# Kernel optimization log

Measured on AMD Instinct MI355X. Metric: run time of the kernel, lower is better.

Reference implementation:

```python
import jax, jax.numpy as jnp
import numpy as np

B, N, D = 2, 2048, 1024
H = 16
HD = D // H


def setup_inputs() -> dict:
    key = jax.random.key(0)
    ks = jax.random.split(key, 10)
    s = 1.0 / np.sqrt(D)
    return {
        "x": jax.random.normal(ks[0], (B, N, D), dtype=jnp.float32),
        "B_gaussian": jax.random.normal(ks[1], (B, N, N), dtype=jnp.float32),
        "Wq": jax.random.normal(ks[2], (D, D), dtype=jnp.float32) * s,
        "bq": jnp.zeros((D,), dtype=jnp.float32),
        "Wk": jax.random.normal(ks[3], (D, D), dtype=jnp.float32) * s,
        "bk": jnp.zeros((D,), dtype=jnp.float32),
        "Wv": jax.random.normal(ks[4], (D, D), dtype=jnp.float32) * s,
        "bv": jnp.zeros((D,), dtype=jnp.float32),
        "Wo": jax.random.normal(ks[5], (D, D), dtype=jnp.float32) * s,
        "bo": jnp.zeros((D,), dtype=jnp.float32),
        "lam": jnp.float32(0.5),
    }


def reference(x, B_gaussian, Wq, bq, Wk, bk, Wv, bv, Wo, bo, lam):
    b, n, d = x.shape
    # project and split heads: [b, h, n, hd]
    def heads(W, bias):
        return (x @ W + bias).reshape(b, n, H, HD).transpose(0, 2, 1, 3)
    q = heads(Wq, bq)
    k = heads(Wk, bk)
    v = heads(Wv, bv)
    scale = 1.0 / np.sqrt(HD)
    # scores [b, h, n, n] with Gaussian bias broadcast across heads
    scores = jnp.einsum("bhid,bhjd->bhij", q, k) * scale + lam * B_gaussian[:, None, :, :]
    w = jax.nn.softmax(scores, axis=-1)
    out = jnp.einsum("bhij,bhjd->bhid", w, v)
    out = out.transpose(0, 2, 1, 3).reshape(b, n, d)
    return out @ Wo + bo
```

## Files before the change

kernel.cpp:

```cpp
#include <hip/hip_runtime.h>
#include <math.h>
#include <stdint.h>

namespace {
constexpr int kB  = 2;
constexpr int kN  = 2048;
constexpr int kD  = 1024;
constexpr int kH  = 16;
constexpr int kM  = kB * kN;
}

typedef __attribute__((ext_vector_type(8))) _Float16 f16x8;
typedef __attribute__((ext_vector_type(2))) __fp16   fp16x2;
typedef __attribute__((ext_vector_type(4))) float    f32x4;

__device__ __forceinline__ void split16(float v, _Float16& h, _Float16& l) {
    h = (_Float16)v;
    l = (_Float16)(v - (float)h);
}

__device__ __forceinline__ void gl2lds16(const _Float16* g, _Float16* l) {
    __builtin_amdgcn_global_load_lds(
        (const __attribute__((address_space(1))) void*)g,
        (__attribute__((address_space(3))) void*)l, 16, 0, 0);
}

__global__ __launch_bounds__(256)
void cvt16(const float* __restrict__ x, _Float16* __restrict__ o)
{
    const size_t i = ((size_t)blockIdx.x * 256 + threadIdx.x) * 8;
    const float4 a = *(const float4*)(x + i);
    const float4 b = *(const float4*)(x + i + 4);
    _Float16 h[8] = {(_Float16)a.x, (_Float16)a.y, (_Float16)a.z, (_Float16)a.w,
                     (_Float16)b.x, (_Float16)b.y, (_Float16)b.z, (_Float16)b.w};
    *(uint4*)(o + i) = *(uint4*)h;
}

__global__ __launch_bounds__(256)
void bgprep(const float* __restrict__ Bg, const float* __restrict__ lam_p,
            _Float16* __restrict__ bgC)
{
    const int t    = blockIdx.x * 256 + threadIdx.x;
    const int lane = t & 63;
    const int i16  = (t >> 6) & 127;
    const int jt   = (t >> 13) & 31;
    const int b    = t >> 18;
    const int q    = lane >> 4;
    const int m    = lane & 15;
    const float c  = lam_p[0] * 8.0f;
    const float* src = Bg + ((size_t)b * kN + i16 * 16 + m) * kN + jt * 64 + q * 4;
    _Float16 h[16];
#pragma unroll
    for (int js = 0; js < 4; ++js) {
        const float4 v = *(const float4*)(src + js * 16);
        h[js * 4 + 0] = (_Float16)(c * v.x);
        h[js * 4 + 1] = (_Float16)(c * v.y);
        h[js * 4 + 2] = (_Float16)(c * v.z);
        h[js * 4 + 3] = (_Float16)(c * v.w);
    }
    _Float16* dst = bgC + (size_t)t * 16;
    *(uint4*)(dst)     = *(uint4*)(h);
    *(uint4*)(dst + 8) = *(uint4*)(h + 8);
}

__global__ __launch_bounds__(256)
void wcvt_t(const float* __restrict__ W, _Float16* __restrict__ Ot)
{
    __shared__ float sT[64][69];
    const int tid = threadIdx.x;
    const int k0 = blockIdx.x << 6;
    const int n0 = blockIdx.y << 6;
#pragma unroll
    for (int rep = 0; rep < 4; ++rep) {
        const int idx = tid + (rep << 8);
        const int kr  = idx >> 4;
        const int c4  = (idx & 15) << 2;
        const float4 v = *(const float4*)(W + (size_t)(k0 + kr) * kD + n0 + c4);
        sT[kr][c4 + 0] = v.x; sT[kr][c4 + 1] = v.y;
        sT[kr][c4 + 2] = v.z; sT[kr][c4 + 3] = v.w;
    }
    __syncthreads();
#pragma unroll
    for (int rep = 0; rep < 2; ++rep) {
        const int slot = tid + (rep << 8);
        const int n  = slot >> 3;
        const int k8 = (slot & 7) << 3;
        _Float16 h8[8];
#pragma unroll
        for (int j = 0; j < 8; ++j) h8[j] = (_Float16)sT[k8 + j][n];
        *(uint4*)(Ot + (size_t)(n0 + n) * kD + k0 + k8) = *(uint4*)h8;
    }
}

__global__ __launch_bounds__(256)
void wsplit_t(const float* __restrict__ W, _Float16* __restrict__ Oh,
              _Float16* __restrict__ Ol)
{
    __shared__ float sT[64][69];
    const int tid = threadIdx.x;
    const int k0 = blockIdx.x << 6;
    const int n0 = blockIdx.y << 6;
#pragma unroll
    for (int rep = 0; rep < 4; ++rep) {
        const int idx = tid + (rep << 8);
        const int kr  = idx >> 4;
        const int c4  = (idx & 15) << 2;
        const float4 v = *(const float4*)(W + (size_t)(k0 + kr) * kD + n0 + c4);
        sT[kr][c4 + 0] = v.x; sT[kr][c4 + 1] = v.y;
        sT[kr][c4 + 2] = v.z; sT[kr][c4 + 3] = v.w;
    }
    __syncthreads();
#pragma unroll
    for (int rep = 0; rep < 2; ++rep) {
        const int slot = tid + (rep << 8);
        const int n  = slot >> 3;
        const int k8 = (slot & 7) << 3;
        _Float16 h8[8], l8[8];
#pragma unroll
        for (int j = 0; j < 8; ++j) split16(sT[k8 + j][n], h8[j], l8[j]);
        *(uint4*)(Oh + (size_t)(n0 + n) * kD + k0 + k8) = *(uint4*)h8;
        *(uint4*)(Ol + (size_t)(n0 + n) * kD + k0 + k8) = *(uint4*)l8;
    }
}

__global__ __launch_bounds__(256)
void gemm16(const _Float16* __restrict__ A, const _Float16* __restrict__ Bt,
            const _Float16* __restrict__ Btl,
            const float* __restrict__ b0, const float* __restrict__ b1,
            const float* __restrict__ b2,
            _Float16* __restrict__ Qf, _Float16* __restrict__ Kf,
            _Float16* __restrict__ Vt, float* __restrict__ outF, int mode)
{
    extern __shared__ _Float16 dyn[];
    _Float16* sA  = dyn;
    _Float16* sB  = dyn + 128 * 64;
    _Float16* sBl = dyn + 2 * 128 * 64;

    const int tid  = threadIdx.x;
    const int lane = tid & 63;
    const int w    = tid >> 6;
    const int quad = lane >> 4;
    const int m16  = lane & 15;
    const int wrow = (w >> 1) << 6;
    const int wcol = (w & 1) << 6;

    const int row0 = blockIdx.y << 7;
    const int col0 = blockIdx.x << 7;

    f32x4 acc[4][4];
#pragma unroll
    for (int mr = 0; mr < 4; ++mr)
#pragma unroll
        for (int nr = 0; nr < 4; ++nr) acc[mr][nr] = (f32x4){0.f, 0.f, 0.f, 0.f};

    const int srl = lane >> 3;
    const int sg  = lane & 7;

    auto stage = [&](const _Float16* gsrc, _Float16* ldst) {
#pragma unroll
        for (int t = 0; t < 4; ++t) {
            const int rr = (w << 5) + (t << 3);
            const int r  = rr + srl;
            const int gg = (sg ^ (r & 7)) << 3;
            gl2lds16(gsrc + (size_t)r * kD + gg, ldst + rr * 64);
        }
    };

    for (int kt = 0; kt < 16; ++kt) {
        const int k0 = kt << 6;
        stage(A  + (size_t)row0 * kD + k0, sA);
        stage(Bt + (size_t)col0 * kD + k0, sB);
        if (mode == 1) stage(Btl + (size_t)col0 * kD + k0, sBl);
        __syncthreads();

#pragma unroll
        for (int ks = 0; ks < 2; ++ks) {
            const int sw = (((ks << 2) | quad) ^ (m16 & 7)) << 3;
            f16x8 af[4], bf[4], blf[4];
#pragma unroll
            for (int mr = 0; mr < 4; ++mr)
                af[mr] = *(const f16x8*)(sA + (wrow + mr * 16 + m16) * 64 + sw);
#pragma unroll
            for (int nr = 0; nr < 4; ++nr) {
                const int off = (wcol + nr * 16 + m16) * 64 + sw;
                bf[nr] = *(const f16x8*)(sB + off);
                if (mode == 1) blf[nr] = *(const f16x8*)(sBl + off);
            }
#pragma unroll
            for (int mr = 0; mr < 4; ++mr)
#pragma unroll
                for (int nr = 0; nr < 4; ++nr) {
                    acc[mr][nr] = __builtin_amdgcn_mfma_f32_16x16x32_f16(af[mr], bf[nr], acc[mr][nr], 0, 0, 0);
                    if (mode == 1)
                        acc[mr][nr] = __builtin_amdgcn_mfma_f32_16x16x32_f16(af[mr], blf[nr], acc[mr][nr], 0, 0, 0);
                }
        }
        __syncthreads();
    }

    if (mode == 1) {
#pragma unroll
        for (int mr = 0; mr < 4; ++mr)
#pragma unroll
            for (int nr = 0; nr < 4; ++nr)
#pragma unroll
                for (int r = 0; r < 4; ++r) {
                    const int row = row0 + wrow + mr * 16 + quad * 4 + r;
                    const int col = col0 + wcol + nr * 16 + m16;
                    outF[(size_t)row * kD + col] = acc[mr][nr][r] + b0[col];
                }
        return;
    }

    const float* bias; int cb; _Float16* dst = nullptr; bool vmode = false;
    if (col0 < 1024)      { bias = b0; cb = col0;        dst = Qf; }
    else if (col0 < 2048) { bias = b1; cb = col0 - 1024; dst = Kf; }
    else                  { bias = b2; cb = col0 - 2048; vmode = true; }

    _Float16* T = dyn;

    if (!vmode) {
#pragma unroll
        for (int mr = 0; mr < 4; ++mr)
#pragma unroll
            for (int nr = 0; nr < 4; ++nr)
#pragma unroll
                for (int r = 0; r < 4; ++r) {
                    const int row = wrow + mr * 16 + quad * 4 + r;
                    const int cl  = wcol + nr * 16 + m16;
                    T[row * 136 + cl] = (_Float16)(acc[mr][nr][r] + bias[cb + cl]);
                }
        __syncthreads();
#pragma unroll
        for (int rep = 0; rep < 8; ++rep) {
            const int slot = tid + (rep << 8);
            const int row = slot >> 4;
            const int c8  = (slot & 15) << 3;
            *(uint4*)(dst + (size_t)(row0 + row) * kD + cb + c8) =
                *(const uint4*)(T + row * 136 + c8);
        }
    } else {
#pragma unroll
        for (int mr = 0; mr < 4; ++mr)
#pragma unroll
            for (int nr = 0; nr < 4; ++nr)
#pragma unroll
                for (int r = 0; r < 4; ++r) {
                    const int tok  = wrow + mr * 16 + quad * 4 + r;
                    const int tokP = (tok & 64) | (tok & 32) |
                                     (((tok >> 2) & 3) << 3) |
                                     (((tok >> 4) & 1) << 2) | (tok & 3);
                    const int cl   = wcol + nr * 16 + m16;
                    T[cl * 136 + tokP] = (_Float16)(acc[mr][nr][r] + bias[cb + cl]);
                }
        __syncthreads();
        const int b  = row0 >> 11;
        const int n0 = row0 & (kN - 1);
#pragma unroll
        for (int rep = 0; rep < 8; ++rep) {
            const int slot = tid + (rep << 8);
            const int cl = slot >> 4;
            const int t8 = (slot & 15) << 3;
            *(uint4*)(Vt + ((size_t)(b * kD + cb + cl)) * kN + n0 + t8) =
                *(const uint4*)(T + cl * 136 + t8);
        }
    }
}

#define STAGE(BUF, S)                                                          \
    {                                                                          \
        const int j0_ = (2 * (S) + grp) << 6;                                  \
        _Float16* kb_ = &sK[grp][BUF][0][0];                                   \
        _Float16* vb_ = &sV[grp][BUF][0][0];                                   \
        _Pragma("unroll")                                                      \
        for (int c_ = 0; c_ < 2; ++c_) {                                       \
            const int rr_ = wg * 16 + c_ * 8;          \
            const int r_  = rr_ + srl;                                         \
            const int gg_ = (sg ^ (r_ & 7)) << 3;       \
            gl2lds16(Kf + (size_t)(b * kN + j0_ + r_) * kD + h * 64 + gg_,     \
                     kb_ + rr_ * 64);                                          \
            gl2lds16(Vt + (size_t)(b * kD + h * 64 + r_) * kN + j0_ + gg_,     \
                     vb_ + rr_ * 64);                                          \
        }                                                                      \
    }

#define LOADBG(S, BG0, BG1, BG2, BG3)                                          \
    {                                                                          \
        const _Float16* bp0_ = bgbase0 + (size_t)(2 * (S) + grp) * kBgJt;      \
        const _Float16* bp1_ = bgbase1 + (size_t)(2 * (S) + grp) * kBgJt;      \
        BG0 = *(const f16x8*)(bp0_);                                           \
        BG1 = *(const f16x8*)(bp0_ + 8);                                       \
        BG2 = *(const f16x8*)(bp1_);                                           \
        BG3 = *(const f16x8*)(bp1_ + 8);                                       \
    }

#define PHASE(BUF, BG0, BG1, BG2, BG3)                                         \
    {                                                                          \
        f32x4 sacc[2][4];                                                      \
        _Pragma("unroll")                                                      \
        for (int r = 0; r < 4; ++r) {                                          \
            sacc[0][0][r] = (float)BG0[r];                                     \
            sacc[0][1][r] = (float)BG0[4 + r];                                 \
            sacc[0][2][r] = (float)BG1[r];                                     \
            sacc[0][3][r] = (float)BG1[4 + r];                                 \
            sacc[1][0][r] = (float)BG2[r];                                     \
            sacc[1][1][r] = (float)BG2[4 + r];                                 \
            sacc[1][2][r] = (float)BG3[r];                                     \
            sacc[1][3][r] = (float)BG3[4 + r];                                 \
        }                                                                      \
        __builtin_amdgcn_s_setprio(1);                                         \
        _Pragma("unroll")                                                      \
        for (int ks = 0; ks < 2; ++ks)                                         \
            _Pragma("unroll")                                                  \
            for (int js = 0; js < 4; ++js) {                                   \
                const int sw_ = ((((ks << 2) | quad)) ^ (m16 & 7)) << 3;       \
                const f16x8 kf = *(const f16x8*)&sK[grp][BUF][js * 16 + m16][sw_];                      \
                sacc[0][js] = __builtin_amdgcn_mfma_f32_16x16x32_f16(kf, qf[0][ks], sacc[0][js], 0, 0, 0); \
                sacc[1][js] = __builtin_amdgcn_mfma_f32_16x16x32_f16(kf, qf[1][ks], sacc[1][js], 0, 0, 0); \
            }                                                                  \
        __builtin_amdgcn_s_setprio(0);                                         \
        union { f16x8 v; unsigned u[4]; } pf[2][2];                            \
        _Pragma("unroll")                                                      \
        for (int iq = 0; iq < 2; ++iq)                                         \
            _Pragma("unroll")                                                  \
            for (int js = 0; js < 4; ++js) {                                   \
                const float p0 = __expf(fmaf(sacc[iq][js][0], 0.125f, -4.0f)); \
                const float p1 = __expf(fmaf(sacc[iq][js][1], 0.125f, -4.0f)); \
                const float p2 = __expf(fmaf(sacc[iq][js][2], 0.125f, -4.0f)); \
                const float p3 = __expf(fmaf(sacc[iq][js][3], 0.125f, -4.0f)); \
                lsum[iq] += (p0 + p1) + (p2 + p3);                             \
                union { fp16x2 h; unsigned u; } ua_, ub_;                      \
                ua_.h = __builtin_amdgcn_cvt_pkrtz(p0, p1);                    \
                ub_.h = __builtin_amdgcn_cvt_pkrtz(p2, p3);                    \
                pf[iq][js >> 1].u[(js & 1) * 2 + 0] = ua_.u;                   \
                pf[iq][js >> 1].u[(js & 1) * 2 + 1] = ub_.u;                   \
            }                                                                  \
        __builtin_amdgcn_s_setprio(1);                                         \
        _Pragma("unroll")                                                      \
        for (int ks = 0; ks < 2; ++ks)                                         \
            _Pragma("unroll")                                                  \
            for (int ds = 0; ds < 4; ++ds) {                                   \
                const int sw_ = ((((ks << 2) | quad)) ^ (m16 & 7)) << 3;       \
                const f16x8 vf = *(const f16x8*)&sV[grp][BUF][ds * 16 + m16][sw_];                      \
                O[0][ds] = __builtin_amdgcn_mfma_f32_16x16x32_f16(pf[0][ks].v, vf, O[0][ds], 0, 0, 0);  \
                O[1][ds] = __builtin_amdgcn_mfma_f32_16x16x32_f16(pf[1][ks].v, vf, O[1][ds], 0, 0, 0);  \
            }                                                                  \
        __builtin_amdgcn_s_setprio(0);                                         \
    }

__global__ __launch_bounds__(512, 2)
void attn_f16(const _Float16* __restrict__ Qf, const _Float16* __restrict__ Kf,
              const _Float16* __restrict__ Vt, const _Float16* __restrict__ BgC,
              _Float16* __restrict__ AOh)
{
    __shared__ _Float16 sK[2][2][64][64];
    __shared__ _Float16 sV[2][2][64][64];

    const int tid  = threadIdx.x;
    const int lane = tid & 63;
    const int w    = tid >> 6;
    const int grp  = w >> 2;
    const int wg   = w & 3;
    const int quad = lane >> 4;
    const int m16  = lane & 15;
    const int srl  = lane >> 3;
    const int sg   = lane & 7;

    const int bh = blockIdx.x;
    const int qt = blockIdx.y;
    const int b  = bh >> 4;
    const int h  = bh & 15;
    const int i0 = qt << 7;

    f16x8 qf[2][2];
#pragma unroll
    for (int iq = 0; iq < 2; ++iq) {
        const size_t qoff =
            (size_t)(b * kN + i0 + iq * 64 + wg * 16 + m16) * kD + h * 64 + quad * 8;
        qf[iq][0] = *(const f16x8*)(Qf + qoff);
        qf[iq][1] = *(const f16x8*)(Qf + qoff + 32);
    }

    f32x4 O[2][4];
#pragma unroll
    for (int iq = 0; iq < 2; ++iq)
#pragma unroll
        for (int ds = 0; ds < 4; ++ds) O[iq][ds] = (f32x4){0.f, 0.f, 0.f, 0.f};
    float lsum[2] = {0.f, 0.f};

    const _Float16* bgbase0 =
        BgC + (((size_t)b * 32 * 128 + (qt * 8 + wg)) * 64 + lane) * 16;
    const _Float16* bgbase1 = bgbase0 + (size_t)4 * 64 * 16;
    constexpr size_t kBgJt = (size_t)128 * 64 * 16;

    f16x8 bgA0, bgA1, bgA2, bgA3, bgB0, bgB1, bgB2, bgB3;

    STAGE(0, 0);
    LOADBG(0, bgA0, bgA1, bgA2, bgA3);
    __syncthreads();

    for (int t = 0; t < 16; t += 2) {
        STAGE(1, t + 1);
        LOADBG(t + 1, bgB0, bgB1, bgB2, bgB3);
        PHASE(0, bgA0, bgA1, bgA2, bgA3);
        __syncthreads();

        if (t + 2 < 16) {
            STAGE(0, t + 2);
            LOADBG(t + 2, bgA0, bgA1, bgA2, bgA3);
        }
        PHASE(1, bgB0, bgB1, bgB2, bgB3);
        __syncthreads();
    }

    const int gtid = tid & 255;
    float* fbuf = (float*)&sK[0][0][0][0];
    if (grp == 1) {
#pragma unroll
        for (int iq = 0; iq < 2; ++iq)
#pragma unroll
            for (int ds = 0; ds < 4; ++ds)
                *(f32x4*)&fbuf[gtid * 36 + (iq * 4 + ds) * 4] = O[iq][ds];
        fbuf[gtid * 36 + 32] = lsum[0];
        fbuf[gtid * 36 + 33] = lsum[1];
    }
    __syncthreads();
    if (grp == 0) {
#pragma unroll
        for (int iq = 0; iq < 2; ++iq) {
#pragma unroll
            for (int ds = 0; ds < 4; ++ds) {
                const f32x4 o2 = *(const f32x4*)&fbuf[gtid * 36 + (iq * 4 + ds) * 4];
                O[iq][ds] += o2;
            }
            lsum[iq] += fbuf[gtid * 36 + 32 + iq];
        }

#pragma unroll
        for (int iq = 0; iq < 2; ++iq) {
            float l = lsum[iq];
            l += __shfl_xor(l, 16, 64);
            l += __shfl_xor(l, 32, 64);

            const int orow = b * kN + i0 + iq * 64 + wg * 16 + quad * 4;
#pragma unroll
            for (int r = 0; r < 4; ++r) {
                const float inv = 1.0f / __shfl(l, quad * 4 + r, 64);
#pragma unroll
                for (int ds = 0; ds < 4; ++ds)
                    AOh[(size_t)(orow + r) * kD + h * 64 + ds * 16 + m16] =
                        (_Float16)(O[iq][ds][r] * inv);
            }
        }
    }
}

extern "C" void kernel_launch(void* const* d_in, const int* in_sizes, int n_in,
                              void* d_out, int out_size, void* d_ws, size_t ws_size,
                              hipStream_t stream)
{
    (void)in_sizes; (void)n_in; (void)out_size; (void)ws_size;

    const float* x   = (const float*)d_in[0];
    const float* Bg  = (const float*)d_in[1];
    const float* Wq  = (const float*)d_in[2];
    const float* bq  = (const float*)d_in[3];
    const float* Wk  = (const float*)d_in[4];
    const float* bk  = (const float*)d_in[5];
    const float* Wv  = (const float*)d_in[6];
    const float* bv  = (const float*)d_in[7];
    const float* Wo  = (const float*)d_in[8];
    const float* bo  = (const float*)d_in[9];
    const float* lam = (const float*)d_in[10];
    float* out = (float*)d_out;
    _Float16* ws16 = (_Float16*)d_ws;

    constexpr size_t kQKV = (size_t)kM * kD;
    constexpr size_t kW   = (size_t)kD * kD;
    _Float16* Qf   = ws16;
    _Float16* Kf   = ws16 + 1 * kQKV;
    _Float16* Vt   = ws16 + 2 * kQKV;
    _Float16* x16  = ws16 + 3 * kQKV;
    _Float16* AOh  = x16;
    _Float16* Wt3  = ws16 + 4 * kQKV;
    _Float16* Woth = Wt3 + 3 * kW;
    _Float16* Wotl = Woth + kW;
    _Float16* BgC  = Wotl + kW;

    dim3 blk(256);

    cvt16<<<dim3(2048), blk, 0, stream>>>(x, x16);
    bgprep<<<dim3(2048), blk, 0, stream>>>(Bg, lam, BgC);
    dim3 wg(kD / 64, kD / 64);
    wcvt_t  <<<wg, blk, 0, stream>>>(Wq, Wt3);
    wcvt_t  <<<wg, blk, 0, stream>>>(Wk, Wt3 + kW);
    wcvt_t  <<<wg, blk, 0, stream>>>(Wv, Wt3 + 2 * kW);
    wsplit_t<<<wg, blk, 0, stream>>>(Wo, Woth, Wotl);

    gemm16<<<dim3(3 * kD / 128, kM / 128), blk, 34816, stream>>>(
        x16, Wt3, nullptr, bq, bk, bv, Qf, Kf, Vt, nullptr, 0);

    attn_f16<<<dim3(kB * kH, kN / 128), dim3(512), 0, stream>>>(
        Qf, Kf, Vt, BgC, AOh);

    gemm16<<<dim3(kD / 128, kM / 128), blk, 49152, stream>>>(
        AOh, Woth, Wotl, bo, nullptr, nullptr,
        nullptr, nullptr, nullptr, out, 1);
}
```

Baseline: 265.2 us.

## Merge prep kernels into one launch and use narrower tiles for output GEMM

Six separate preprocessing kernels (x conversion, bias scaling, three weight transposes, Wo hi/lo split) are merged into a single launch that dispatches on block index, cutting launch overhead and gaps between kernels. The output projection moves from the mode-switched gemm16 to a dedicated kernel with 128x64 tiles. That doubles the grid from 256 to 512 blocks to fill more CUs, and drops the runtime mode branches from the QKV GEMM. The cost is less reuse of the A tile per block in the output GEMM.

```diff
diff --git a/kernel.cpp b/kernel.cpp
--- a/kernel.cpp
+++ b/kernel.cpp
@@ -8,6 +8,7 @@
 constexpr int kD  = 1024;
 constexpr int kH  = 16;
 constexpr int kM  = kB * kN;
+constexpr size_t kW = (size_t)kD * kD;
 }
 
 typedef __attribute__((ext_vector_type(8))) _Float16 f16x8;
@@ -26,50 +27,60 @@
 }
 
 __global__ __launch_bounds__(256)
-void cvt16(const float* __restrict__ x, _Float16* __restrict__ o)
-{
-    const size_t i = ((size_t)blockIdx.x * 256 + threadIdx.x) * 8;
-    const float4 a = *(const float4*)(x + i);
-    const float4 b = *(const float4*)(x + i + 4);
-    _Float16 h[8] = {(_Float16)a.x, (_Float16)a.y, (_Float16)a.z, (_Float16)a.w,
-                     (_Float16)b.x, (_Float16)b.y, (_Float16)b.z, (_Float16)b.w};
-    *(uint4*)(o + i) = *(uint4*)h;
-}
-
-__global__ __launch_bounds__(256)
-void bgprep(const float* __restrict__ Bg, const float* __restrict__ lam_p,
-            _Float16* __restrict__ bgC)
-{
-    const int t    = blockIdx.x * 256 + threadIdx.x;
-    const int lane = t & 63;
-    const int i16  = (t >> 6) & 127;
-    const int jt   = (t >> 13) & 31;
-    const int b    = t >> 18;
-    const int q    = lane >> 4;
-    const int m    = lane & 15;
-    const float c  = lam_p[0] * 8.0f;
-    const float* src = Bg + ((size_t)b * kN + i16 * 16 + m) * kN + jt * 64 + q * 4;
-    _Float16 h[16];
-#pragma unroll
-    for (int js = 0; js < 4; ++js) {
-        const float4 v = *(const float4*)(src + js * 16);
-        h[js * 4 + 0] = (_Float16)(c * v.x);
-        h[js * 4 + 1] = (_Float16)(c * v.y);
-        h[js * 4 + 2] = (_Float16)(c * v.z);
-        h[js * 4 + 3] = (_Float16)(c * v.w);
-    }
-    _Float16* dst = bgC + (size_t)t * 16;
-    *(uint4*)(dst)     = *(uint4*)(h);
-    *(uint4*)(dst + 8) = *(uint4*)(h + 8);
-}
-
-__global__ __launch_bounds__(256)
-void wcvt_t(const float* __restrict__ W, _Float16* __restrict__ Ot)
+void prep_all(const float* __restrict__ x, const float* __restrict__ Bg,
+              const float* __restrict__ lam_p,
+              const float* __restrict__ Wq, const float* __restrict__ Wk,
+              const float* __restrict__ Wv, const float* __restrict__ Wo,
+              _Float16* __restrict__ x16, _Float16* __restrict__ bgC,
+              _Float16* __restrict__ Wt3, _Float16* __restrict__ Woh,
+              _Float16* __restrict__ Wol)
 {
     __shared__ float sT[64][69];
+    const int bx  = blockIdx.x;
     const int tid = threadIdx.x;
-    const int k0 = blockIdx.x << 6;
-    const int n0 = blockIdx.y << 6;
+
+    if (bx < 2048) {
+        const size_t i = ((size_t)bx * 256 + tid) * 8;
+        const float4 a = *(const float4*)(x + i);
+        const float4 b = *(const float4*)(x + i + 4);
+        _Float16 h[8] = {(_Float16)a.x, (_Float16)a.y, (_Float16)a.z, (_Float16)a.w,
+                         (_Float16)b.x, (_Float16)b.y, (_Float16)b.z, (_Float16)b.w};
+        *(uint4*)(x16 + i) = *(uint4*)h;
+        return;
+    }
+
+    if (bx < 4096) {
+        const int t    = (bx - 2048) * 256 + tid;
+        const int lane = t & 63;
+        const int i16  = (t >> 6) & 127;
+        const int jt   = (t >> 13) & 31;
+        const int b    = t >> 18;
+        const int q    = lane >> 4;
+        const int m    = lane & 15;
+        const float c  = lam_p[0] * 8.0f;
+        const float* src = Bg + ((size_t)b * kN + i16 * 16 + m) * kN + jt * 64 + q * 4;
+        _Float16 h[16];
+#pragma unroll
+        for (int js = 0; js < 4; ++js) {
+            const float4 v = *(const float4*)(src + js * 16);
+            h[js * 4 + 0] = (_Float16)(c * v.x);
+            h[js * 4 + 1] = (_Float16)(c * v.y);
+            h[js * 4 + 2] = (_Float16)(c * v.z);
+            h[js * 4 + 3] = (_Float16)(c * v.w);
+        }
+        _Float16* dst = bgC + (size_t)t * 16;
+        *(uint4*)(dst)     = *(uint4*)(h);
+        *(uint4*)(dst + 8) = *(uint4*)(h + 8);
+        return;
+    }
+
+    const int local = bx - 4096;
+    const int which = local >> 8;
+    const int wi    = local & 255;
+    const int k0 = (wi & 15) << 6;
+    const int n0 = (wi >> 4) << 6;
+    const float* W = (which == 0) ? Wq : (which == 1) ? Wk : (which == 2) ? Wv : Wo;
+
 #pragma unroll
     for (int rep = 0; rep < 4; ++rep) {
         const int idx = tid + (rep << 8);
@@ -80,61 +91,44 @@
         sT[kr][c4 + 2] = v.z; sT[kr][c4 + 3] = v.w;
     }
     __syncthreads();
-#pragma unroll
-    for (int rep = 0; rep < 2; ++rep) {
-        const int slot = tid + (rep << 8);
-        const int n  = slot >> 3;
-        const int k8 = (slot & 7) << 3;
-        _Float16 h8[8];
-#pragma unroll
-        for (int j = 0; j < 8; ++j) h8[j] = (_Float16)sT[k8 + j][n];
-        *(uint4*)(Ot + (size_t)(n0 + n) * kD + k0 + k8) = *(uint4*)h8;
-    }
-}
-
-__global__ __launch_bounds__(256)
-void wsplit_t(const float* __restrict__ W, _Float16* __restrict__ Oh,
-              _Float16* __restrict__ Ol)
-{
-    __shared__ float sT[64][69];
-    const int tid = threadIdx.x;
-    const int k0 = blockIdx.x << 6;
-    const int n0 = blockIdx.y << 6;
-#pragma unroll
-    for (int rep = 0; rep < 4; ++rep) {
-        const int idx = tid + (rep << 8);
-        const int kr  = idx >> 4;
-        const int c4  = (idx & 15) << 2;
-        const float4 v = *(const float4*)(W + (size_t)(k0 + kr) * kD + n0 + c4);
-        sT[kr][c4 + 0] = v.x; sT[kr][c4 + 1] = v.y;
-        sT[kr][c4 + 2] = v.z; sT[kr][c4 + 3] = v.w;
-    }
-    __syncthreads();
-#pragma unroll
-    for (int rep = 0; rep < 2; ++rep) {
-        const int slot = tid + (rep << 8);
-        const int n  = slot >> 3;
-        const int k8 = (slot & 7) << 3;
-        _Float16 h8[8], l8[8];
-#pragma unroll
-        for (int j = 0; j < 8; ++j) split16(sT[k8 + j][n], h8[j], l8[j]);
-        *(uint4*)(Oh + (size_t)(n0 + n) * kD + k0 + k8) = *(uint4*)h8;
-        *(uint4*)(Ol + (size_t)(n0 + n) * kD + k0 + k8) = *(uint4*)l8;
+
+    if (which < 3) {
+        _Float16* Ot = Wt3 + (size_t)which * kW;
+#pragma unroll
+        for (int rep = 0; rep < 2; ++rep) {
+            const int slot = tid + (rep << 8);
+            const int n  = slot >> 3;
+            const int k8 = (slot & 7) << 3;
+            _Float16 h8[8];
+#pragma unroll
+            for (int j = 0; j < 8; ++j) h8[j] = (_Float16)sT[k8 + j][n];
+            *(uint4*)(Ot + (size_t)(n0 + n) * kD + k0 + k8) = *(uint4*)h8;
+        }
+    } else {
+#pragma unroll
+        for (int rep = 0; rep < 2; ++rep) {
+            const int slot = tid + (rep << 8);
+            const int n  = slot >> 3;
+            const int k8 = (slot & 7) << 3;
+            _Float16 h8[8], l8[8];
+#pragma unroll
+            for (int j = 0; j < 8; ++j) split16(sT[k8 + j][n], h8[j], l8[j]);
+            *(uint4*)(Woh + (size_t)(n0 + n) * kD + k0 + k8) = *(uint4*)h8;
+            *(uint4*)(Wol + (size_t)(n0 + n) * kD + k0 + k8) = *(uint4*)l8;
+        }
     }
 }
 
 __global__ __launch_bounds__(256)
 void gemm16(const _Float16* __restrict__ A, const _Float16* __restrict__ Bt,
-            const _Float16* __restrict__ Btl,
             const float* __restrict__ b0, const float* __restrict__ b1,
             const float* __restrict__ b2,
             _Float16* __restrict__ Qf, _Float16* __restrict__ Kf,
-            _Float16* __restrict__ Vt, float* __restrict__ outF, int mode)
+            _Float16* __restrict__ Vt)
 {
     extern __shared__ _Float16 dyn[];
     _Float16* sA  = dyn;
     _Float16* sB  = dyn + 128 * 64;
-    _Float16* sBl = dyn + 2 * 128 * 64;
 
     const int tid  = threadIdx.x;
     const int lane = tid & 63;
@@ -170,46 +164,25 @@
         const int k0 = kt << 6;
         stage(A  + (size_t)row0 * kD + k0, sA);
         stage(Bt + (size_t)col0 * kD + k0, sB);
-        if (mode == 1) stage(Btl + (size_t)col0 * kD + k0, sBl);
         __syncthreads();
 
 #pragma unroll
         for (int ks = 0; ks < 2; ++ks) {
             const int sw = (((ks << 2) | quad) ^ (m16 & 7)) << 3;
-            f16x8 af[4], bf[4], blf[4];
+            f16x8 af[4], bf[4];
 #pragma unroll
             for (int mr = 0; mr < 4; ++mr)
                 af[mr] = *(const f16x8*)(sA + (wrow + mr * 16 + m16) * 64 + sw);
 #pragma unroll
-            for (int nr = 0; nr < 4; ++nr) {
-                const int off = (wcol + nr * 16 + m16) * 64 + sw;
-                bf[nr] = *(const f16x8*)(sB + off);
-                if (mode == 1) blf[nr] = *(const f16x8*)(sBl + off);
-            }
+            for (int nr = 0; nr < 4; ++nr)
+                bf[nr] = *(const f16x8*)(sB + (wcol + nr * 16 + m16) * 64 + sw);
 #pragma unroll
             for (int mr = 0; mr < 4; ++mr)
 #pragma unroll
-                for (int nr = 0; nr < 4; ++nr) {
+                for (int nr = 0; nr < 4; ++nr)
                     acc[mr][nr] = __builtin_amdgcn_mfma_f32_16x16x32_f16(af[mr], bf[nr], acc[mr][nr], 0, 0, 0);
-                    if (mode == 1)
-                        acc[mr][nr] = __builtin_amdgcn_mfma_f32_16x16x32_f16(af[mr], blf[nr], acc[mr][nr], 0, 0, 0);
-                }
-        }
-        __syncthreads();
-    }
-
-    if (mode == 1) {
-#pragma unroll
-        for (int mr = 0; mr < 4; ++mr)
-#pragma unroll
-            for (int nr = 0; nr < 4; ++nr)
-#pragma unroll
-                for (int r = 0; r < 4; ++r) {
-                    const int row = row0 + wrow + mr * 16 + quad * 4 + r;
-                    const int col = col0 + wcol + nr * 16 + m16;
-                    outF[(size_t)row * kD + col] = acc[mr][nr][r] + b0[col];
-                }
-        return;
+        }
+        __syncthreads();
     }
 
     const float* bias; int cb; _Float16* dst = nullptr; bool vmode = false;
@@ -265,6 +238,89 @@
                 *(const uint4*)(T + cl * 136 + t8);
         }
     }
+}
+
+__global__ __launch_bounds__(256)
+void gemmOut(const _Float16* __restrict__ A, const _Float16* __restrict__ Bth,
+             const _Float16* __restrict__ Btl, const float* __restrict__ bias,
+             float* __restrict__ outF)
+{
+    __shared__ _Float16 sA[128][64];
+    __shared__ _Float16 sBh[64][64];
+    __shared__ _Float16 sBl[64][64];
+
+    const int tid  = threadIdx.x;
+    const int lane = tid & 63;
+    const int w    = tid >> 6;
+    const int quad = lane >> 4;
+    const int m16  = lane & 15;
+    const int wrow = (w >> 1) << 6;
+    const int wcol = (w & 1) << 5;
+
+    const int row0 = blockIdx.y << 7;
+    const int col0 = blockIdx.x << 6;
+
+    const int srl = lane >> 3;
+    const int sg  = lane & 7;
+
+    f32x4 acc[4][2];
+#pragma unroll
+    for (int mr = 0; mr < 4; ++mr)
+#pragma unroll
+        for (int nr = 0; nr < 2; ++nr) acc[mr][nr] = (f32x4){0.f, 0.f, 0.f, 0.f};
+
+    for (int kt = 0; kt < 16; ++kt) {
+        const int k0 = kt << 6;
+#pragma unroll
+        for (int t = 0; t < 4; ++t) {
+            const int rr = (w << 5) + (t << 3);
+            const int r  = rr + srl;
+            const int gg = (sg ^ (r & 7)) << 3;
+            gl2lds16(A + (size_t)(row0 + r) * kD + k0 + gg, &sA[0][0] + rr * 64);
+        }
+#pragma unroll
+        for (int t = 0; t < 2; ++t) {
+            const int rr = (w << 4) + (t << 3);
+            const int r  = rr + srl;
+            const int gg = (sg ^ (r & 7)) << 3;
+            gl2lds16(Bth + (size_t)(col0 + r) * kD + k0 + gg, &sBh[0][0] + rr * 64);
+            gl2lds16(Btl + (size_t)(col0 + r) * kD + k0 + gg, &sBl[0][0] + rr * 64);
+        }
+        __syncthreads();
+
+#pragma unroll
+        for (int ks = 0; ks < 2; ++ks) {
+            const int sw = (((ks << 2) | quad) ^ (m16 & 7)) << 3;
+            f16x8 af[4], bh[2], bl[2];
+#pragma unroll
+            for (int mr = 0; mr < 4; ++mr)
+                af[mr] = *(const f16x8*)(&sA[0][0] + (wrow + mr * 16 + m16) * 64 + sw);
+#pragma unroll
+            for (int nr = 0; nr < 2; ++nr) {
+                bh[nr] = *(const f16x8*)(&sBh[0][0] + (wcol + nr * 16 + m16) * 64 + sw);
+                bl[nr] = *(const f16x8*)(&sBl[0][0] + (wcol + nr * 16 + m16) * 64 + sw);
+            }
+#pragma unroll
+            for (int mr = 0; mr < 4; ++mr)
+#pragma unroll
+                for (int nr = 0; nr < 2; ++nr) {
+                    acc[mr][nr] = __builtin_amdgcn_mfma_f32_16x16x32_f16(af[mr], bh[nr], acc[mr][nr], 0, 0, 0);
+                    acc[mr][nr] = __builtin_amdgcn_mfma_f32_16x16x32_f16(af[mr], bl[nr], acc[mr][nr], 0, 0, 0);
+                }
+        }
+        __syncthreads();
+    }
+
+#pragma unroll
+    for (int mr = 0; mr < 4; ++mr)
+#pragma unroll
+        for (int nr = 0; nr < 2; ++nr)
+#pragma unroll
+            for (int r = 0; r < 4; ++r) {
+                const int row = row0 + wrow + mr * 16 + quad * 4 + r;
+                const int col = col0 + wcol + nr * 16 + m16;
+                outF[(size_t)row * kD + col] = acc[mr][nr][r] + bias[col];
+            }
 }
 
 #define STAGE(BUF, S)                                                          \
@@ -476,7 +532,6 @@
     _Float16* ws16 = (_Float16*)d_ws;
 
     constexpr size_t kQKV = (size_t)kM * kD;
-    constexpr size_t kW   = (size_t)kD * kD;
     _Float16* Qf   = ws16;
     _Float16* Kf   = ws16 + 1 * kQKV;
     _Float16* Vt   = ws16 + 2 * kQKV;
@@ -487,23 +542,15 @@
     _Float16* Wotl = Woth + kW;
     _Float16* BgC  = Wotl + kW;
 
-    dim3 blk(256);
-
-    cvt16<<<dim3(2048), blk, 0, stream>>>(x, x16);
-    bgprep<<<dim3(2048), blk, 0, stream>>>(Bg, lam, BgC);
-    dim3 wg(kD / 64, kD / 64);
-    wcvt_t  <<<wg, blk, 0, stream>>>(Wq, Wt3);
-    wcvt_t  <<<wg, blk, 0, stream>>>(Wk, Wt3 + kW);
-    wcvt_t  <<<wg, blk, 0, stream>>>(Wv, Wt3 + 2 * kW);
-    wsplit_t<<<wg, blk, 0, stream>>>(Wo, Woth, Wotl);
-
-    gemm16<<<dim3(3 * kD / 128, kM / 128), blk, 34816, stream>>>(
-        x16, Wt3, nullptr, bq, bk, bv, Qf, Kf, Vt, nullptr, 0);
+    prep_all<<<dim3(5120), dim3(256), 0, stream>>>(
+        x, Bg, lam, Wq, Wk, Wv, Wo, x16, BgC, Wt3, Woth, Wotl);
+
+    gemm16<<<dim3(3 * kD / 128, kM / 128), dim3(256), 34816, stream>>>(
+        x16, Wt3, bq, bk, bv, Qf, Kf, Vt);
 
     attn_f16<<<dim3(kB * kH, kN / 128), dim3(512), 0, stream>>>(
         Qf, Kf, Vt, BgC, AOh);
 
-    gemm16<<<dim3(kD / 128, kM / 128), blk, 49152, stream>>>(
-        AOh, Woth, Wotl, bo, nullptr, nullptr,
-        nullptr, nullptr, nullptr, out, 1);
-}
+    gemmOut<<<dim3(kD / 64, kM / 128), dim3(256), 0, stream>>>(
+        AOh, Woth, Wotl, bo, out);
+}
```

Measured after the change: 238.5 us. 10.1% less time.
